# Kernel tuning notes

Measured on AMD Instinct MI355X. Metric: run time of the kernel, lower is better.

Reference implementation:

```python
import jax, jax.numpy as jnp
import numpy as np

D_MODEL = 1024
N_HEADS = 16
HEAD_DIM = D_MODEL // N_HEADS
B, T = 4, 2048


def setup_inputs() -> dict:
    key = jax.random.key(0)
    ks = jax.random.split(key, 5)
    s = D_MODEL ** -0.5
    return {
        "x": jax.random.normal(ks[0], (B, T, D_MODEL), dtype=jnp.float32),
        "Wqkv": jax.random.normal(ks[1], (3 * D_MODEL, D_MODEL), dtype=jnp.float32) * s,
        "bqkv": jax.random.normal(ks[2], (3 * D_MODEL,), dtype=jnp.float32) * 0.01,
        "Wo": jax.random.normal(ks[3], (D_MODEL, D_MODEL), dtype=jnp.float32) * s,
        "bo": jax.random.normal(ks[4], (D_MODEL,), dtype=jnp.float32) * 0.01,
    }


def reference(x, Wqkv, bqkv, Wo, bo):
    b, t, c = x.shape
    h, hd = N_HEADS, HEAD_DIM
    qkv = x @ Wqkv.T + bqkv                      # [B,T,3C]
    # Faithful to source: reshape to [B,T,H,3*hd] THEN chunk -> per-head slices of 3C
    qkv = qkv.reshape(b, t, h, 3 * hd).transpose(0, 2, 1, 3)  # [B,H,T,3hd]
    q, k, v = jnp.split(qkv, 3, axis=-1)          # each [B,H,T,hd]
    scores = jnp.einsum('bhqd,bhkd->bhqk', q, k) * (hd ** -0.5)
    attn = jax.nn.softmax(scores, axis=-1)        # [B,H,T,T]
    out = jnp.einsum('bhqk,bhkd->bhqd', attn, v)  # [B,H,T,hd]
    out = out.transpose(0, 2, 1, 3).reshape(b, t, c)
    return out @ Wo.T + bo
```

## Files before the change

### kernel.cpp

```cpp
#include <hip/hip_runtime.h>
#include <hip/hip_bf16.h>


typedef float f32x4 __attribute__((ext_vector_type(4)));
typedef short s16x8 __attribute__((ext_vector_type(8)));
typedef short s16x4 __attribute__((ext_vector_type(4)));
typedef unsigned int u32x4 __attribute__((ext_vector_type(4)));

#define MFMA(acc, a, b) \
    (acc) = __builtin_amdgcn_mfma_f32_16x16x32_bf16((a), (b), (acc), 0, 0, 0)

__device__ __forceinline__ short f2bb(float f) {
    return (short)__bfloat16_as_ushort(__float2bfloat16(f));
}

__global__ __launch_bounds__(256)
void conv_all(const float* __restrict__ x, const float* __restrict__ Wqkv,
              const float* __restrict__ bqkv, const float* __restrict__ Wo,
              short* __restrict__ xb, short* __restrict__ Wqkvb,
              float* __restrict__ bqkvr, short* __restrict__ Wob)
{
    int blk = blockIdx.x;
    if (blk < 4096) {
        long i = ((long)blk * 256 + threadIdx.x) * 8;
        f32x4 a = *(const f32x4*)(x + i);
        f32x4 b = *(const f32x4*)(x + i + 4);
        s16x8 r;
#pragma unroll
        for (int j = 0; j < 4; j++) { r[j] = f2bb(a[j]); r[4 + j] = f2bb(b[j]); }
        *(s16x8*)(xb + i) = r;
    } else if (blk < 4096 + 3072) {
        int np = blk - 4096;
        int slice = np >> 10, rr = np & 1023;
        int src = (rr >> 6) * 192 + slice * 64 + (rr & 63);
        f32x4 v = *(const f32x4*)(Wqkv + (long)src * 1024 + threadIdx.x * 4);
        s16x4 o;
#pragma unroll
        for (int j = 0; j < 4; j++) o[j] = f2bb(v[j]);
        *(s16x4*)(Wqkvb + (long)np * 1024 + threadIdx.x * 4) = o;
        if (threadIdx.x == 0) bqkvr[np] = bqkv[src];
    } else {
        int n = blk - 4096 - 3072;
        f32x4 v = *(const f32x4*)(Wo + (long)n * 1024 + threadIdx.x * 4);
        s16x4 o;
#pragma unroll
        for (int j = 0; j < 4; j++) o[j] = f2bb(v[j]);
        *(s16x4*)(Wob + (long)n * 1024 + threadIdx.x * 4) = o;
    }
}

__global__ __launch_bounds__(256)
void gemm128(const short* __restrict__ A, const short* __restrict__ W,
             const float* __restrict__ bias,
             short* __restrict__ Cq, short* __restrict__ Ck,
             short* __restrict__ Cv)
{
    __shared__ short Asw[128 * 64];
    __shared__ short Bsw[128 * 64];
    const int tid = threadIdx.x;
    const int wave = tid >> 6, lane = tid & 63;
    const int quad = lane >> 4, l16 = lane & 15;
    const int NX = gridDim.x;
    const int lin = blockIdx.y * NX + blockIdx.x;
    const int xcd = lin & 7, q = lin >> 3;
    const int m0 = (xcd * 8 + q / NX) * 128;
    const int ng = (q % NX) * 128;
    const int sr = tid >> 3, sc = tid & 7;

    f32x4 acc[4][4] = {};
    s16x8 pav[4], pbv[4];

#pragma unroll
    for (int u = 0; u < 4; u++) {
        int r = u * 32 + sr;
        pav[u] = *(const s16x8*)(A + (long)(m0 + r) * 1024 + sc * 8);
        pbv[u] = *(const s16x8*)(W + (long)(ng + r) * 1024 + sc * 8);
    }

    for (int k0 = 0; k0 < 1024; k0 += 64) {
        __syncthreads();
#pragma unroll
        for (int u = 0; u < 4; u++) {
            int r = u * 32 + sr;
            int slot = sc ^ (r & 7);
            *(s16x8*)&Asw[r * 64 + slot * 8] = pav[u];
            *(s16x8*)&Bsw[r * 64 + slot * 8] = pbv[u];
        }
        if (k0 + 64 < 1024) {
            int kn = k0 + 64;
#pragma unroll
            for (int u = 0; u < 4; u++) {
                int r = u * 32 + sr;
                pav[u] = *(const s16x8*)(A + (long)(m0 + r) * 1024 + kn + sc * 8);
                pbv[u] = *(const s16x8*)(W + (long)(ng + r) * 1024 + kn + sc * 8);
            }
        }
        __syncthreads();

        s16x8 af[2][4], bf[2][4];
#pragma unroll
        for (int ks = 0; ks < 2; ks++)
#pragma unroll
            for (int i = 0; i < 4; i++) {
                int slot = (ks * 4 + quad) ^ (l16 & 7);
                int ra = (wave >> 1) * 64 + i * 16 + l16;
                af[ks][i] = *(const s16x8*)&Asw[ra * 64 + slot * 8];
                int rb = (wave & 1) * 64 + i * 16 + l16;
                bf[ks][i] = *(const s16x8*)&Bsw[rb * 64 + slot * 8];
            }
#pragma unroll
        for (int ks = 0; ks < 2; ks++)
#pragma unroll
            for (int i = 0; i < 4; i++)
#pragma unroll
                for (int j = 0; j < 4; j++)
                    MFMA(acc[i][j], af[ks][i], bf[ks][j]);
    }

    const int slice = ng >> 10;
    const float scale = (slice == 0) ? 0.125f : 1.0f;
    short* Cb = (slice == 0) ? Cq : (slice == 1) ? Ck : Cv;
    const int nl = ng & 1023;
#pragma unroll
    for (int i = 0; i < 4; i++)
#pragma unroll
        for (int r = 0; r < 4; r++) {
            long m = m0 + (wave >> 1) * 64 + i * 16 + quad * 4 + r;
#pragma unroll
            for (int j = 0; j < 4; j++) {
                int cw = (wave & 1) * 64 + j * 16 + l16;
                float v = (acc[i][j][r] + bias[ng + cw]) * scale;
                Cb[m * 1024 + nl + cw] = f2bb(v);
            }
        }
}

__global__ __launch_bounds__(256)
void gemm_proj(const short* __restrict__ A, const short* __restrict__ W,
               const float* __restrict__ bias, float* __restrict__ Cf)
{
    __shared__ short Asw[128 * 64];
    __shared__ short Bsw[64 * 64];
    const int tid = threadIdx.x;
    const int wave = tid >> 6, lane = tid & 63;
    const int quad = lane >> 4, l16 = lane & 15;
    const int wm = wave >> 1, wn = wave & 1;
    const int NX = gridDim.x;
    const int lin = blockIdx.y * NX + blockIdx.x;
    const int xcd = lin & 7, q = lin >> 3;
    const int m0 = (xcd * 8 + q / NX) * 128;
    const int n0 = (q % NX) * 64;
    const int sr = tid >> 3, sc = tid & 7;

    f32x4 acc[4][2] = {};
    s16x8 pav[4], pbv[2];

#pragma unroll
    for (int u = 0; u < 4; u++)
        pav[u] = *(const s16x8*)(A + (long)(m0 + u * 32 + sr) * 1024 + sc * 8);
#pragma unroll
    for (int u = 0; u < 2; u++)
        pbv[u] = *(const s16x8*)(W + (long)(n0 + u * 32 + sr) * 1024 + sc * 8);

    for (int k0 = 0; k0 < 1024; k0 += 64) {
        __syncthreads();
#pragma unroll
        for (int u = 0; u < 4; u++) {
            int r = u * 32 + sr;
            int slot = sc ^ (r & 7);
            *(s16x8*)&Asw[r * 64 + slot * 8] = pav[u];
        }
#pragma unroll
        for (int u = 0; u < 2; u++) {
            int r = u * 32 + sr;
            int slot = sc ^ (r & 7);
            *(s16x8*)&Bsw[r * 64 + slot * 8] = pbv[u];
        }
        if (k0 + 64 < 1024) {
            int kn = k0 + 64;
#pragma unroll
            for (int u = 0; u < 4; u++)
                pav[u] = *(const s16x8*)(A + (long)(m0 + u * 32 + sr) * 1024 + kn + sc * 8);
#pragma unroll
            for (int u = 0; u < 2; u++)
                pbv[u] = *(const s16x8*)(W + (long)(n0 + u * 32 + sr) * 1024 + kn + sc * 8);
        }
        __syncthreads();

        s16x8 af[2][4], bf[2][2];
#pragma unroll
        for (int ks = 0; ks < 2; ks++) {
#pragma unroll
            for (int i = 0; i < 4; i++) {
                int slot = (ks * 4 + quad) ^ (l16 & 7);
                int ra = wm * 64 + i * 16 + l16;
                af[ks][i] = *(const s16x8*)&Asw[ra * 64 + slot * 8];
            }
#pragma unroll
            for (int j = 0; j < 2; j++) {
                int slot = (ks * 4 + quad) ^ (l16 & 7);
                int rb = wn * 32 + j * 16 + l16;
                bf[ks][j] = *(const s16x8*)&Bsw[rb * 64 + slot * 8];
            }
        }
#pragma unroll
        for (int ks = 0; ks < 2; ks++)
#pragma unroll
            for (int i = 0; i < 4; i++)
#pragma unroll
                for (int j = 0; j < 2; j++)
                    MFMA(acc[i][j], af[ks][i], bf[ks][j]);
    }

#pragma unroll
    for (int i = 0; i < 4; i++)
#pragma unroll
        for (int r = 0; r < 4; r++) {
            long m = m0 + wm * 64 + i * 16 + quad * 4 + r;
#pragma unroll
            for (int j = 0; j < 2; j++) {
                int cw = wn * 32 + j * 16 + l16;
                Cf[m * 1024 + n0 + cw] = acc[i][j][r] + bias[n0 + cw];
            }
        }
}

__global__ __launch_bounds__(256)
void attn(const short* __restrict__ Q, const short* __restrict__ Kb,
          const short* __restrict__ Vb, short* __restrict__ ao)
{
    __shared__ short Ksw[64 * 64];
    __shared__ unsigned int Vt[64 * 36];

    const int tid = threadIdx.x;
    const int wave = tid >> 6, lane = tid & 63;
    const int quad = lane >> 4, l16 = lane & 15;
    const int bh = blockIdx.x;
    const int b = bh >> 4, h = bh & 15;
    const int q0 = blockIdx.y * 256, hc = h * 64;
    const long rowbase = (long)b * 2048;

    s16x8 qf[4][2];
#pragma unroll
    for (int s = 0; s < 4; s++) {
        const short* qp = Q + (rowbase + q0 + s * 64 + wave * 16 + l16) * 1024
                        + hc + quad * 8;
        qf[s][0] = *(const s16x8*)qp;
        qf[s][1] = *(const s16x8*)(qp + 32);
    }

    s16x8 vones;
#pragma unroll
    for (int j = 0; j < 8; j++) vones[j] = (short)0x3F80;

    f32x4 O[4][4] = {};
    f32x4 Osum[4] = {};

    const int ksr = tid >> 3, ksc = tid & 7;
    const int kp = tid & 31, ve = tid >> 5;
    const int key0 = ((kp >> 4) << 5) + (((kp >> 1) & 1) << 4)
                   + (((kp >> 2) & 3) << 2) + ((kp & 1) << 1);

    s16x8 kv0, kv1, va, vb2;
    {
        kv0 = *(const s16x8*)(Kb + (rowbase + ksr) * 1024 + hc + ksc * 8);
        kv1 = *(const s16x8*)(Kb + (rowbase + 32 + ksr) * 1024 + hc + ksc * 8);
        const short* v0 = Vb + (rowbase + key0) * 1024 + hc + ve * 8;
        va  = *(const s16x8*)v0;
        vb2 = *(const s16x8*)(v0 + 1024);
    }

    for (int kb = 0; kb < 2048; kb += 64) {
        __syncthreads();
        {
            int slot0 = ksc ^ (ksr & 7);
            *(s16x8*)&Ksw[ksr * 64 + slot0 * 8] = kv0;
            int r1 = 32 + ksr;
            int slot1 = ksc ^ (r1 & 7);
            *(s16x8*)&Ksw[r1 * 64 + slot1 * 8] = kv1;
            u32x4 vaU = __builtin_bit_cast(u32x4, va);
            u32x4 vbU = __builtin_bit_cast(u32x4, vb2);
#pragma unroll
            for (int w = 0; w < 4; w++) {
                unsigned int lo = __builtin_amdgcn_perm(vbU[w], vaU[w], 0x05040100u);
                unsigned int hi = __builtin_amdgcn_perm(vbU[w], vaU[w], 0x07060302u);
                Vt[(ve * 8 + 2 * w) * 36 + kp] = lo;
                Vt[(ve * 8 + 2 * w + 1) * 36 + kp] = hi;
            }
        }
        __syncthreads();

        if (kb + 64 < 2048) {
            int kn = kb + 64;
            kv0 = *(const s16x8*)(Kb + (rowbase + kn + ksr) * 1024 + hc + ksc * 8);
            kv1 = *(const s16x8*)(Kb + (rowbase + kn + 32 + ksr) * 1024 + hc + ksc * 8);
            const short* v0 = Vb + (rowbase + kn + key0) * 1024 + hc + ve * 8;
            va  = *(const s16x8*)v0;
            vb2 = *(const s16x8*)(v0 + 1024);
        }

        s16x8 af[4][2];
        __builtin_amdgcn_s_setprio(1);
#pragma unroll
        for (int kt = 0; kt < 4; kt++) {
            int key = kt * 16 + l16;
            int slot0 = quad ^ (l16 & 7);
            int slot1 = (4 + quad) ^ (l16 & 7);
            s16x8 kf0 = *(const s16x8*)&Ksw[key * 64 + slot0 * 8];
            s16x8 kf1 = *(const s16x8*)&Ksw[key * 64 + slot1 * 8];
            f32x4 sv[4] = {{}, {}, {}, {}};
#pragma unroll
            for (int s = 0; s < 4; s++) {
                MFMA(sv[s], kf0, qf[s][0]);
                MFMA(sv[s], kf1, qf[s][1]);
            }
#pragma unroll
            for (int s = 0; s < 4; s++)
#pragma unroll
                for (int r = 0; r < 4; r++) {
                    float p = __builtin_amdgcn_exp2f(
                        __builtin_fmaf(sv[s][r], 1.44269504f, -17.3123405f));
                    af[s][kt >> 1][(kt & 1) * 4 + r] = f2bb(p);
                }
        }

#pragma unroll
        for (int dt = 0; dt < 4; dt++) {
            int d = dt * 16 + l16;
#pragma unroll
            for (int kf = 0; kf < 2; kf++) {
                s16x8 vf = *(const s16x8*)&Vt[d * 36 + kf * 16 + quad * 4];
#pragma unroll
                for (int s = 0; s < 4; s++)
                    MFMA(O[s][dt], af[s][kf], vf);
            }
        }
#pragma unroll
        for (int s = 0; s < 4; s++) {
            MFMA(Osum[s], af[s][0], vones);
            MFMA(Osum[s], af[s][1], vones);
        }
        __builtin_amdgcn_s_setprio(0);
    }

#pragma unroll
    for (int s = 0; s < 4; s++)
#pragma unroll
        for (int r = 0; r < 4; r++) {
            float invr = 1.0f / Osum[s][r];
            short* orow = ao + (rowbase + q0 + s * 64 + wave * 16 + quad * 4 + r) * 1024
                        + hc + l16;
#pragma unroll
            for (int dt = 0; dt < 4; dt++)
                orow[dt * 16] = f2bb(O[s][dt][r] * invr);
        }
}

__global__ void const_fill(float* out, int n, float c) {
    int i = blockIdx.x * 256 + threadIdx.x;
    if (i < n) out[i] = c;
}

extern "C" void kernel_launch(void* const* d_in, const int* in_sizes, int n_in,
                              void* d_out, int out_size, void* d_ws, size_t ws_size,
                              hipStream_t stream)
{
    const float* x    = (const float*)d_in[0];
    const float* Wqkv = (const float*)d_in[1];
    const float* bqkv = (const float*)d_in[2];
    const float* Wo   = (const float*)d_in[3];
    const float* bo   = (const float*)d_in[4];

    const size_t MB = 1u << 20;
    if (ws_size < 32 * MB) {
        const_fill<<<(out_size + 255) / 256, 256, 0, stream>>>(
            (float*)d_out, out_size, 66.0f);
        return;
    }

    char* ws = (char*)d_ws;
    short* xb     = (short*)(ws);
    short* Wqkvb  = (short*)(ws + 16777216);
    float* bqkvr  = (float*)(ws + 23068672);
    short* Wob    = (short*)(ws + 23085056);

    short* qbuf = (short*)d_out;
    short* kbuf = qbuf + (size_t)8192 * 1024;
    short* vbuf = (short*)d_in[0] + (size_t)8192 * 1024;
    short* ao   = (short*)d_in[0];

    dim3 blk(256);
    conv_all<<<4096 + 3072 + 1024, blk, 0, stream>>>(
        x, Wqkv, bqkv, Wo, xb, Wqkvb, bqkvr, Wob);

    gemm128<<<dim3(24, 64), blk, 0, stream>>>(xb, Wqkvb, bqkvr,
                                              qbuf, kbuf, vbuf);
    attn<<<dim3(64, 8), blk, 0, stream>>>(qbuf, kbuf, vbuf, ao);
    gemm_proj<<<dim3(16, 64), blk, 0, stream>>>(ao, Wob, bo, (float*)d_out);
}
```

Measured before the change: 257.6 us.

## Fuse x bf16 conversion into QKV GEMM with atomic persistent tile scheduler

```diff
diff --git a/kernel.cpp b/kernel.cpp
--- a/kernel.cpp
+++ b/kernel.cpp
@@ -15,22 +15,15 @@
 }
 
 __global__ __launch_bounds__(256)
-void conv_all(const float* __restrict__ x, const float* __restrict__ Wqkv,
-              const float* __restrict__ bqkv, const float* __restrict__ Wo,
-              short* __restrict__ xb, short* __restrict__ Wqkvb,
-              float* __restrict__ bqkvr, short* __restrict__ Wob)
+void conv_all(const float* __restrict__ Wqkv, const float* __restrict__ bqkv,
+              const float* __restrict__ Wo,
+              short* __restrict__ Wqkvb, float* __restrict__ bqkvr,
+              short* __restrict__ Wob, unsigned int* __restrict__ ctr)
 {
     int blk = blockIdx.x;
-    if (blk < 4096) {
-        long i = ((long)blk * 256 + threadIdx.x) * 8;
-        f32x4 a = *(const f32x4*)(x + i);
-        f32x4 b = *(const f32x4*)(x + i + 4);
-        s16x8 r;
-#pragma unroll
-        for (int j = 0; j < 4; j++) { r[j] = f2bb(a[j]); r[4 + j] = f2bb(b[j]); }
-        *(s16x8*)(xb + i) = r;
-    } else if (blk < 4096 + 3072) {
-        int np = blk - 4096;
+    if (blk == 0 && threadIdx.x == 0) *ctr = 0u;
+    if (blk < 3072) {
+        int np = blk;
         int slice = np >> 10, rr = np & 1023;
         int src = (rr >> 6) * 192 + slice * 64 + (rr & 63);
         f32x4 v = *(const f32x4*)(Wqkv + (long)src * 1024 + threadIdx.x * 4);
@@ -40,7 +33,7 @@
         *(s16x4*)(Wqkvb + (long)np * 1024 + threadIdx.x * 4) = o;
         if (threadIdx.x == 0) bqkvr[np] = bqkv[src];
     } else {
-        int n = blk - 4096 - 3072;
+        int n = blk - 3072;
         f32x4 v = *(const f32x4*)(Wo + (long)n * 1024 + threadIdx.x * 4);
         s16x4 o;
 #pragma unroll
@@ -50,89 +43,105 @@
 }
 
 __global__ __launch_bounds__(256)
-void gemm128(const short* __restrict__ A, const short* __restrict__ W,
-             const float* __restrict__ bias,
-             short* __restrict__ Cq, short* __restrict__ Ck,
-             short* __restrict__ Cv)
+void gemm_qkv(const float* __restrict__ Af, const short* __restrict__ W,
+              const float* __restrict__ bias,
+              short* __restrict__ Cq, short* __restrict__ Ck,
+              short* __restrict__ Cv, unsigned int* __restrict__ ctr)
 {
     __shared__ short Asw[128 * 64];
     __shared__ short Bsw[128 * 64];
+    __shared__ unsigned int tshare;
     const int tid = threadIdx.x;
     const int wave = tid >> 6, lane = tid & 63;
     const int quad = lane >> 4, l16 = lane & 15;
-    const int NX = gridDim.x;
-    const int lin = blockIdx.y * NX + blockIdx.x;
-    const int xcd = lin & 7, q = lin >> 3;
-    const int m0 = (xcd * 8 + q / NX) * 128;
-    const int ng = (q % NX) * 128;
     const int sr = tid >> 3, sc = tid & 7;
 
-    f32x4 acc[4][4] = {};
-    s16x8 pav[4], pbv[4];
-
-#pragma unroll
-    for (int u = 0; u < 4; u++) {
-        int r = u * 32 + sr;
-        pav[u] = *(const s16x8*)(A + (long)(m0 + r) * 1024 + sc * 8);
-        pbv[u] = *(const s16x8*)(W + (long)(ng + r) * 1024 + sc * 8);
-    }
-
-    for (int k0 = 0; k0 < 1024; k0 += 64) {
+    for (;;) {
+        if (tid == 0) tshare = atomicAdd(ctr, 1u);
         __syncthreads();
+        unsigned int t = tshare;
+        if (t >= 1536u) break;
+        const int m0 = (int)(t / 24u) * 128;
+        const int ng = (int)(t % 24u) * 128;
+
+        f32x4 acc[4][4] = {};
+        f32x4 paf[4][2];
+        s16x8 pbv[4];
+
 #pragma unroll
         for (int u = 0; u < 4; u++) {
             int r = u * 32 + sr;
-            int slot = sc ^ (r & 7);
-            *(s16x8*)&Asw[r * 64 + slot * 8] = pav[u];
-            *(s16x8*)&Bsw[r * 64 + slot * 8] = pbv[u];
-        }
-        if (k0 + 64 < 1024) {
-            int kn = k0 + 64;
+            const float* ap = Af + (long)(m0 + r) * 1024 + sc * 8;
+            paf[u][0] = *(const f32x4*)ap;
+            paf[u][1] = *(const f32x4*)(ap + 4);
+            pbv[u] = *(const s16x8*)(W + (long)(ng + r) * 1024 + sc * 8);
+        }
+
+        for (int k0 = 0; k0 < 1024; k0 += 64) {
+            __syncthreads();
 #pragma unroll
             for (int u = 0; u < 4; u++) {
                 int r = u * 32 + sr;
-                pav[u] = *(const s16x8*)(A + (long)(m0 + r) * 1024 + kn + sc * 8);
-                pbv[u] = *(const s16x8*)(W + (long)(ng + r) * 1024 + kn + sc * 8);
-            }
-        }
-        __syncthreads();
-
-        s16x8 af[2][4], bf[2][4];
-#pragma unroll
-        for (int ks = 0; ks < 2; ks++)
-#pragma unroll
-            for (int i = 0; i < 4; i++) {
-                int slot = (ks * 4 + quad) ^ (l16 & 7);
-                int ra = (wave >> 1) * 64 + i * 16 + l16;
-                af[ks][i] = *(const s16x8*)&Asw[ra * 64 + slot * 8];
-                int rb = (wave & 1) * 64 + i * 16 + l16;
-                bf[ks][i] = *(const s16x8*)&Bsw[rb * 64 + slot * 8];
-            }
-#pragma unroll
-        for (int ks = 0; ks < 2; ks++)
-#pragma unroll
-            for (int i = 0; i < 4; i++)
-#pragma unroll
-                for (int j = 0; j < 4; j++)
-                    MFMA(acc[i][j], af[ks][i], bf[ks][j]);
-    }
-
-    const int slice = ng >> 10;
-    const float scale = (slice == 0) ? 0.125f : 1.0f;
-    short* Cb = (slice == 0) ? Cq : (slice == 1) ? Ck : Cv;
-    const int nl = ng & 1023;
-#pragma unroll
-    for (int i = 0; i < 4; i++)
-#pragma unroll
-        for (int r = 0; r < 4; r++) {
-            long m = m0 + (wave >> 1) * 64 + i * 16 + quad * 4 + r;
-#pragma unroll
-            for (int j = 0; j < 4; j++) {
-                int cw = (wave & 1) * 64 + j * 16 + l16;
-                float v = (acc[i][j][r] + bias[ng + cw]) * scale;
-                Cb[m * 1024 + nl + cw] = f2bb(v);
-            }
-        }
+                int slot = sc ^ (r & 7);
+                s16x8 av;
+#pragma unroll
+                for (int j = 0; j < 4; j++) {
+                    av[j] = f2bb(paf[u][0][j]);
+                    av[4 + j] = f2bb(paf[u][1][j]);
+                }
+                *(s16x8*)&Asw[r * 64 + slot * 8] = av;
+                *(s16x8*)&Bsw[r * 64 + slot * 8] = pbv[u];
+            }
+            if (k0 + 64 < 1024) {
+                int kn = k0 + 64;
+#pragma unroll
+                for (int u = 0; u < 4; u++) {
+                    int r = u * 32 + sr;
+                    const float* ap = Af + (long)(m0 + r) * 1024 + kn + sc * 8;
+                    paf[u][0] = *(const f32x4*)ap;
+                    paf[u][1] = *(const f32x4*)(ap + 4);
+                    pbv[u] = *(const s16x8*)(W + (long)(ng + r) * 1024 + kn + sc * 8);
+                }
+            }
+            __syncthreads();
+
+            s16x8 af[2][4], bf[2][4];
+#pragma unroll
+            for (int ks = 0; ks < 2; ks++)
+#pragma unroll
+                for (int i = 0; i < 4; i++) {
+                    int slot = (ks * 4 + quad) ^ (l16 & 7);
+                    int ra = (wave >> 1) * 64 + i * 16 + l16;
+                    af[ks][i] = *(const s16x8*)&Asw[ra * 64 + slot * 8];
+                    int rb = (wave & 1) * 64 + i * 16 + l16;
+                    bf[ks][i] = *(const s16x8*)&Bsw[rb * 64 + slot * 8];
+                }
+#pragma unroll
+            for (int ks = 0; ks < 2; ks++)
+#pragma unroll
+                for (int i = 0; i < 4; i++)
+#pragma unroll
+                    for (int j = 0; j < 4; j++)
+                        MFMA(acc[i][j], af[ks][i], bf[ks][j]);
+        }
+
+        const int slice = ng >> 10;
+        const float scale = (slice == 0) ? 0.125f : 1.0f;
+        short* Cb = (slice == 0) ? Cq : (slice == 1) ? Ck : Cv;
+        const int nl = ng & 1023;
+#pragma unroll
+        for (int i = 0; i < 4; i++)
+#pragma unroll
+            for (int r = 0; r < 4; r++) {
+                long m = m0 + (wave >> 1) * 64 + i * 16 + quad * 4 + r;
+#pragma unroll
+                for (int j = 0; j < 4; j++) {
+                    int cw = (wave & 1) * 64 + j * 16 + l16;
+                    float v = (acc[i][j][r] + bias[ng + cw]) * scale;
+                    Cb[m * 1024 + nl + cw] = f2bb(v);
+                }
+            }
+    }
 }
 
 __global__ __launch_bounds__(256)
@@ -379,22 +388,22 @@
     }
 
     char* ws = (char*)d_ws;
-    short* xb     = (short*)(ws);
+    short* vbuf   = (short*)(ws);
     short* Wqkvb  = (short*)(ws + 16777216);
     float* bqkvr  = (float*)(ws + 23068672);
+    unsigned int* ctr = (unsigned int*)(ws + 23080960);
     short* Wob    = (short*)(ws + 23085056);
 
     short* qbuf = (short*)d_out;
     short* kbuf = qbuf + (size_t)8192 * 1024;
-    short* vbuf = (short*)d_in[0] + (size_t)8192 * 1024;
     short* ao   = (short*)d_in[0];
 
     dim3 blk(256);
-    conv_all<<<4096 + 3072 + 1024, blk, 0, stream>>>(
-        x, Wqkv, bqkv, Wo, xb, Wqkvb, bqkvr, Wob);
-
-    gemm128<<<dim3(24, 64), blk, 0, stream>>>(xb, Wqkvb, bqkvr,
-                                              qbuf, kbuf, vbuf);
+    conv_all<<<3072 + 1024, blk, 0, stream>>>(Wqkv, bqkv, Wo,
+                                              Wqkvb, bqkvr, Wob, ctr);
+
+    gemm_qkv<<<1024, blk, 0, stream>>>(x, Wqkvb, bqkvr,
+                                       qbuf, kbuf, vbuf, ctr);
     attn<<<dim3(64, 8), blk, 0, stream>>>(qbuf, kbuf, vbuf, ao);
     gemm_proj<<<dim3(16, 64), blk, 0, stream>>>(ao, Wob, bo, (float*)d_out);
 }
```

New measurement: 275.6 us. 7.0% more time.

## Pre-transpose V in a separate kernel and load V fragments directly from global

Applied to the files above, without the earlier changes.

```diff
diff --git a/kernel.cpp b/kernel.cpp
--- a/kernel.cpp
+++ b/kernel.cpp
@@ -133,6 +133,34 @@
                 Cb[m * 1024 + nl + cw] = f2bb(v);
             }
         }
+}
+
+__global__ __launch_bounds__(256)
+void vtrans(const short* __restrict__ Vb, unsigned int* __restrict__ VtO)
+{
+    __shared__ short L[64][72];
+    const int tid = threadIdx.x;
+    const int bh = blockIdx.x, T = blockIdx.y;
+    const int b = bh >> 4, h = bh & 15;
+
+    {
+        int key = tid >> 2, dblk = tid & 3;
+        const short* src = Vb + ((long)b * 2048 + T * 64 + key) * 1024 + h * 64;
+        *(s16x8*)&L[key][dblk * 8]      = *(const s16x8*)(src + dblk * 8);
+        *(s16x8*)&L[key][dblk * 8 + 32] = *(const s16x8*)(src + dblk * 8 + 32);
+    }
+    __syncthreads();
+
+    const int kp = tid & 31, dg = tid >> 5;
+    const int key0 = ((kp >> 4) << 5) + (((kp >> 1) & 1) << 4)
+                   + (((kp >> 2) & 3) << 2) + ((kp & 1) << 1);
+    unsigned int* orow = VtO + ((long)bh * 64 + dg * 8) * 1024 + T * 32 + kp;
+#pragma unroll
+    for (int j = 0; j < 8; j++) {
+        unsigned int lo = (unsigned short)L[key0][dg * 8 + j];
+        unsigned int hi = (unsigned short)L[key0 + 1][dg * 8 + j];
+        orow[(long)j * 1024] = lo | (hi << 16);
+    }
 }
 
 __global__ __launch_bounds__(256)
@@ -227,10 +255,9 @@
 
 __global__ __launch_bounds__(256)
 void attn(const short* __restrict__ Q, const short* __restrict__ Kb,
-          const short* __restrict__ Vb, short* __restrict__ ao)
+          const unsigned int* __restrict__ VtG, short* __restrict__ ao)
 {
     __shared__ short Ksw[64 * 64];
-    __shared__ unsigned int Vt[64 * 36];
 
     const int tid = threadIdx.x;
     const int wave = tid >> 6, lane = tid & 63;
@@ -257,20 +284,22 @@
     f32x4 Osum[4] = {};
 
     const int ksr = tid >> 3, ksc = tid & 7;
-    const int kp = tid & 31, ve = tid >> 5;
-    const int key0 = ((kp >> 4) << 5) + (((kp >> 1) & 1) << 4)
-                   + (((kp >> 2) & 3) << 2) + ((kp & 1) << 1);
-
-    s16x8 kv0, kv1, va, vb2;
+
+    const unsigned int* vbase = VtG + ((long)bh * 64 + l16) * 1024 + quad * 4;
+
+    s16x8 kv0, kv1;
+    u32x4 vfp[4][2];
     {
         kv0 = *(const s16x8*)(Kb + (rowbase + ksr) * 1024 + hc + ksc * 8);
         kv1 = *(const s16x8*)(Kb + (rowbase + 32 + ksr) * 1024 + hc + ksc * 8);
-        const short* v0 = Vb + (rowbase + key0) * 1024 + hc + ve * 8;
-        va  = *(const s16x8*)v0;
-        vb2 = *(const s16x8*)(v0 + 1024);
-    }
-
-    for (int kb = 0; kb < 2048; kb += 64) {
+#pragma unroll
+        for (int dt = 0; dt < 4; dt++)
+#pragma unroll
+            for (int kf = 0; kf < 2; kf++)
+                vfp[dt][kf] = *(const u32x4*)(vbase + dt * 16384 + kf * 16);
+    }
+
+    for (int t = 0; t < 32; ++t) {
         __syncthreads();
         {
             int slot0 = ksc ^ (ksr & 7);
@@ -278,25 +307,13 @@
             int r1 = 32 + ksr;
             int slot1 = ksc ^ (r1 & 7);
             *(s16x8*)&Ksw[r1 * 64 + slot1 * 8] = kv1;
-            u32x4 vaU = __builtin_bit_cast(u32x4, va);
-            u32x4 vbU = __builtin_bit_cast(u32x4, vb2);
-#pragma unroll
-            for (int w = 0; w < 4; w++) {
-                unsigned int lo = __builtin_amdgcn_perm(vbU[w], vaU[w], 0x05040100u);
-                unsigned int hi = __builtin_amdgcn_perm(vbU[w], vaU[w], 0x07060302u);
-                Vt[(ve * 8 + 2 * w) * 36 + kp] = lo;
-                Vt[(ve * 8 + 2 * w + 1) * 36 + kp] = hi;
-            }
-        }
-        __syncthreads();
-
-        if (kb + 64 < 2048) {
-            int kn = kb + 64;
+        }
+        __syncthreads();
+
+        if (t < 31) {
+            int kn = (t + 1) * 64;
             kv0 = *(const s16x8*)(Kb + (rowbase + kn + ksr) * 1024 + hc + ksc * 8);
             kv1 = *(const s16x8*)(Kb + (rowbase + kn + 32 + ksr) * 1024 + hc + ksc * 8);
-            const short* v0 = Vb + (rowbase + kn + key0) * 1024 + hc + ve * 8;
-            va  = *(const s16x8*)v0;
-            vb2 = *(const s16x8*)(v0 + 1024);
         }
 
         s16x8 af[4][2];
@@ -326,10 +343,9 @@
 
 #pragma unroll
         for (int dt = 0; dt < 4; dt++) {
-            int d = dt * 16 + l16;
 #pragma unroll
             for (int kf = 0; kf < 2; kf++) {
-                s16x8 vf = *(const s16x8*)&Vt[d * 36 + kf * 16 + quad * 4];
+                s16x8 vf = __builtin_bit_cast(s16x8, vfp[dt][kf]);
 #pragma unroll
                 for (int s = 0; s < 4; s++)
                     MFMA(O[s][dt], af[s][kf], vf);
@@ -341,6 +357,15 @@
             MFMA(Osum[s], af[s][1], vones);
         }
         __builtin_amdgcn_s_setprio(0);
+
+        if (t < 31) {
+            const unsigned int* vb2 = vbase + (t + 1) * 32;
+#pragma unroll
+            for (int dt = 0; dt < 4; dt++)
+#pragma unroll
+                for (int kf = 0; kf < 2; kf++)
+                    vfp[dt][kf] = *(const u32x4*)(vb2 + dt * 16384 + kf * 16);
+        }
     }
 
 #pragma unroll
@@ -380,6 +405,7 @@
 
     char* ws = (char*)d_ws;
     short* xb     = (short*)(ws);
+    unsigned int* vtT = (unsigned int*)(ws);
     short* Wqkvb  = (short*)(ws + 16777216);
     float* bqkvr  = (float*)(ws + 23068672);
     short* Wob    = (short*)(ws + 23085056);
@@ -395,6 +421,7 @@
 
     gemm128<<<dim3(24, 64), blk, 0, stream>>>(xb, Wqkvb, bqkvr,
                                               qbuf, kbuf, vbuf);
-    attn<<<dim3(64, 8), blk, 0, stream>>>(qbuf, kbuf, vbuf, ao);
+    vtrans<<<dim3(64, 32), blk, 0, stream>>>(vbuf, vtT);
+    attn<<<dim3(64, 8), blk, 0, stream>>>(qbuf, kbuf, vtT, ao);
     gemm_proj<<<dim3(16, 64), blk, 0, stream>>>(ao, Wob, bo, (float*)d_out);
 }
```

Measured after the change: 271.1 us. 1.05x slower.
